# Optimization experiments

Hardware: AMD Instinct MI355X
Metric: run time of the kernel (lower is better)

Reference implementation:

```python
import jax, jax.numpy as jnp
import numpy as np

NUM_HEADS = 16


def _apply_rotary(x, cos, sin):
    # x: [B, H, L, D]; cos/sin: [L, D//2] broadcast over B, H
    d = x.shape[-1] // 2
    x1, x2 = x[..., :d], x[..., d:]
    return jnp.concatenate([x1 * cos - x2 * sin, x2 * cos + x1 * sin], axis=-1)


def setup_inputs() -> dict:
    key = jax.random.key(0)
    k_x, k_c, k_s, k_qkv, k_w, k_b = jax.random.split(key, 6)
    B, L, dim = 2, 2048, 2048
    head_dim = dim // NUM_HEADS
    x = jax.random.normal(k_x, (B, L, dim), dtype=jnp.float32)
    cos = jax.random.uniform(k_c, (L, head_dim // 2), dtype=jnp.float32)
    sin = jax.random.uniform(k_s, (L, head_dim // 2), dtype=jnp.float32)
    scale = 1.0 / np.sqrt(dim)
    w_qkv = jax.random.normal(k_qkv, (dim, 3 * dim), dtype=jnp.float32) * scale
    w_out = jax.random.normal(k_w, (dim, dim), dtype=jnp.float32) * scale
    b_out = jax.random.normal(k_b, (dim,), dtype=jnp.float32) * 0.01
    return {"x": x, "cos": cos, "sin": sin, "w_qkv": w_qkv, "w_out": w_out, "b_out": b_out}


def reference(x, cos, sin, w_qkv, w_out, b_out):
    B, L, dim = x.shape
    H = NUM_HEADS
    D = dim // H
    # fused QKV projection (no bias), split to q,k,v: [B, H, L, D]
    qkv = (x @ w_qkv).reshape(B, L, 3, H, D)
    qkv = jnp.transpose(qkv, (2, 0, 3, 1, 4))
    q, k, v = qkv[0], qkv[1], qkv[2]
    q = _apply_rotary(q, cos, sin)
    k = _apply_rotary(k, cos, sin)
    # scaled dot-product attention (non-causal, scale = 1/sqrt(D))
    scores = jnp.einsum('bhqd,bhkd->bhqk', q, k) / jnp.sqrt(jnp.asarray(D, q.dtype))
    attn = jax.nn.softmax(scores, axis=-1)
    out = jnp.einsum('bhqk,bhkd->bhqd', attn, v)  # [B, H, L, D]
    out = jnp.transpose(out, (0, 2, 1, 3)).reshape(B, L, dim)
    return out @ w_out + b_out
```

## Files before the change

kernel.cpp:

```cpp
#include <hip/hip_runtime.h>
#include <cstdint>
#include <cstddef>

typedef unsigned short u16;
typedef __attribute__((ext_vector_type(2))) unsigned short u16x2;
typedef __attribute__((ext_vector_type(4))) unsigned short u16x4;
typedef __attribute__((ext_vector_type(8))) unsigned short u16x8;
typedef __attribute__((ext_vector_type(4))) float f32x4;
typedef __attribute__((ext_vector_type(8))) __bf16 bf16x8;

#define B_    2
#define L_    2048
#define DIM_  2048
#define H_    16
#define HD_   128
#define NQKV_ 6144
#define M_    4096

__device__ __forceinline__ float b2f(u16 h) {
  union { unsigned u; float f; } v; v.u = ((unsigned)h) << 16; return v.f;
}
__device__ __forceinline__ u16 f2bf(float f) {
  unsigned u = __float_as_uint(f);
  u += 0x7fffu + ((u >> 16) & 1u);
  return (u16)(u >> 16);
}
__device__ __forceinline__ f32x4 mfma16(bf16x8 a, bf16x8 b, f32x4 c) {
  return __builtin_amdgcn_mfma_f32_16x16x32_bf16(a, b, c, 0, 0, 0);
}
__device__ __forceinline__ void async16(const void* g, void* l) {
  __builtin_amdgcn_global_load_lds(
      (const __attribute__((address_space(1))) unsigned*)g,
      (__attribute__((address_space(3))) unsigned*)l, 16, 0, 0);
}

__global__ __launch_bounds__(256) void cvt_bf16(
    const float* __restrict__ src, u16* __restrict__ dst) {
  int i = (blockIdx.x * 256 + threadIdx.x) * 4;
  f32x4 v = *(const f32x4*)&src[i];
  u16x4 o;
  #pragma unroll
  for (int j = 0; j < 4; ++j) o[j] = f2bf(v[j]);
  *(u16x4*)&dst[i] = o;
}

__global__ __launch_bounds__(256) void transpose_cvt(
    const float* __restrict__ src, u16* __restrict__ dst, int R, int C) {
  __shared__ u16 tile[64][66];
  int r0 = blockIdx.y * 64, c0 = blockIdx.x * 64;
  #pragma unroll
  for (int i = 0; i < 16; ++i) {
    int f = i * 256 + threadIdx.x;
    int r = f >> 6, c = f & 63;
    tile[r][c] = f2bf(src[(size_t)(r0 + r) * C + (c0 + c)]);
  }
  __syncthreads();
  #pragma unroll
  for (int i = 0; i < 8; ++i) {
    int f = i * 256 + threadIdx.x;
    int cr = f >> 5, rp = (f & 31) * 2;
    u16x2 v = {tile[rp][cr], tile[rp + 1][cr]};
    *(u16x2*)&dst[(size_t)(c0 + cr) * R + (r0 + rp)] = v;
  }
}

template <int MODE>
__global__ __launch_bounds__(256) void gemm_bt(
    const u16* __restrict__ A, const u16* __restrict__ Bt,
    u16* __restrict__ D0, u16* __restrict__ D1, u16* __restrict__ D2,
    const float* __restrict__ bias, float* __restrict__ outp,
    int M, int N, int K) {
  __shared__ __align__(16) u16 Alds[128 * 32];
  __shared__ __align__(16) u16 Blds[128 * 32];
  const int tid = threadIdx.x;
  const int wave = tid >> 6, lane = tid & 63;
  const int wm = wave >> 1, wn = wave & 1;
  const int ln = lane & 15, qd = lane >> 4;
  const int m0 = blockIdx.y * 128, n0 = blockIdx.x * 128;

  f32x4 acc[4][4];
  #pragma unroll
  for (int i = 0; i < 4; ++i)
    #pragma unroll
    for (int j = 0; j < 4; ++j) acc[i][j] = (f32x4){0.f, 0.f, 0.f, 0.f};

  for (int k0 = 0; k0 < K; k0 += 32) {
    __syncthreads();
    #pragma unroll
    for (int j = 0; j < 2; ++j) {
      int f = (j * 256 + tid) * 8;
      int r = f >> 5, c = f & 31;
      async16(&A[(size_t)(m0 + r) * K + (k0 + c)], &Alds[j * 2048 + wave * 512]);
      async16(&Bt[(size_t)(n0 + r) * K + (k0 + c)], &Blds[j * 2048 + wave * 512]);
    }
    __syncthreads();
    bf16x8 af[4], bfr[4];
    #pragma unroll
    for (int mi = 0; mi < 4; ++mi)
      af[mi] = *(const bf16x8*)&Alds[(wm * 64 + mi * 16 + ln) * 32 + qd * 8];
    #pragma unroll
    for (int ni = 0; ni < 4; ++ni)
      bfr[ni] = *(const bf16x8*)&Blds[(wn * 64 + ni * 16 + ln) * 32 + qd * 8];
    #pragma unroll
    for (int mi = 0; mi < 4; ++mi)
      #pragma unroll
      for (int ni = 0; ni < 4; ++ni)
        acc[mi][ni] = mfma16(af[mi], bfr[ni], acc[mi][ni]);
  }

  #pragma unroll
  for (int mi = 0; mi < 4; ++mi) {
    #pragma unroll
    for (int ni = 0; ni < 4; ++ni) {
      #pragma unroll
      for (int r = 0; r < 4; ++r) {
        int row = m0 + wm * 64 + mi * 16 + qd * 4 + r;
        int col = n0 + wn * 64 + ni * 16 + ln;
        float v = acc[mi][ni][r];
        if (MODE == 2) {
          outp[(size_t)row * N + col] = v + bias[col];
        } else {
          int t = col >> 11;
          int hc = col & 2047;
          int h = hc >> 7, d = hc & 127;
          int b = row >> 11, l = row & 2047;
          u16* dst = (t == 0) ? D0 : ((t == 1) ? D1 : D2);
          dst[((size_t)(b * H_ + h) * L_ + l) * HD_ + d] = f2bf(v);
        }
      }
    }
  }
}

__global__ __launch_bounds__(128) void rotary_k(
    u16* __restrict__ Q, u16* __restrict__ Kb,
    const float* __restrict__ cs, const float* __restrict__ sn) {
  int bid = blockIdx.x;
  int l = bid & (L_ - 1);
  int t = threadIdx.x;
  int d = t & 63;
  u16* P = (t < 64) ? Q : Kb;
  size_t base = (size_t)bid * HD_;
  int ci = l * 64 + d;
  float c = cs[ci], s = sn[ci];
  float x1 = b2f(P[base + d]), x2 = b2f(P[base + d + 64]);
  P[base + d] = f2bf(x1 * c - x2 * s);
  P[base + d + 64] = f2bf(x2 * c + x1 * s);
}

__global__ __launch_bounds__(256) void attn_k(
    const u16* __restrict__ Q, const u16* __restrict__ Kb,
    const u16* __restrict__ V, u16* __restrict__ Ao) {
  __shared__ __align__(16) u16 lds[26624];
  u16* Klds = lds;
  u16* Vlds = lds + 8192;
  u16* Plds = lds + 17408;
  const int tid = threadIdx.x;
  const int w = tid >> 6, lane = tid & 63;
  const int ln = lane & 15, qd = lane >> 4;
  const int qt = blockIdx.x, bh = blockIdx.y;
  const int b = bh >> 4, h = bh & 15;
  const size_t slab = (size_t)bh * (L_ * HD_);
  const int vp = tid & 63, vd0 = 2 * vp;

  #pragma unroll
  for (int j = 0; j < 8; ++j) {
    int oe = j * 2048 + w * 512 + lane * 8;
    int se = oe ^ (((oe >> 7) & 7) << 3);
    async16(&Q[slab + (size_t)qt * 16384 + se], &lds[j * 2048 + w * 512]);
  }
  __syncthreads();
  bf16x8 aq[2][4];
  #pragma unroll
  for (int mi = 0; mi < 2; ++mi) {
    int qrow = w * 32 + mi * 16 + ln;
    #pragma unroll
    for (int kc = 0; kc < 4; ++kc)
      aq[mi][kc] = *(const bf16x8*)&lds[qrow * 128 +
                                        ((kc * 32 + qd * 8) ^ ((qrow & 7) << 3))];
  }

  f32x4 o[2][8];
  #pragma unroll
  for (int i = 0; i < 2; ++i)
    #pragma unroll
    for (int j = 0; j < 8; ++j) o[i][j] = (f32x4){0.f, 0.f, 0.f, 0.f};
  float mst[2][4], lst[2][4];
  #pragma unroll
  for (int i = 0; i < 2; ++i)
    #pragma unroll
    for (int r = 0; r < 4; ++r) { mst[i][r] = -1e30f; lst[i][r] = 0.f; }
  const float SC = 0.12751744f;

  for (int it = 0; it < 32; ++it) {
    unsigned vv[2][8];
    #pragma unroll
    for (int n2 = 0; n2 < 2; ++n2) {
      int key0 = ((tid >> 6) + n2 * 4) * 8;
      #pragma unroll
      for (int e = 0; e < 8; ++e)
        vv[n2][e] = *(const unsigned*)&V[slab + (size_t)(it * 64 + key0 + e) * 128 + vd0];
    }
    __syncthreads();
    #pragma unroll
    for (int j = 0; j < 4; ++j) {
      int oe = j * 2048 + w * 512 + lane * 8;
      int se = oe ^ (((oe >> 7) & 7) << 3);
      async16(&Kb[slab + (size_t)it * 8192 + se], &Klds[j * 2048 + w * 512]);
    }
    #pragma unroll
    for (int n2 = 0; n2 < 2; ++n2) {
      int key0 = ((tid >> 6) + n2 * 4) * 8;
      u16x8 lo, hi;
      #pragma unroll
      for (int e = 0; e < 8; ++e) {
        lo[e] = (u16)(vv[n2][e] & 0xffffu);
        hi[e] = (u16)(vv[n2][e] >> 16);
      }
      *(u16x8*)&Vlds[vd0 * 72 + key0] = lo;
      *(u16x8*)&Vlds[(vd0 + 1) * 72 + key0] = hi;
    }
    __syncthreads();

    f32x4 sa[2][4];
    #pragma unroll
    for (int i = 0; i < 2; ++i)
      #pragma unroll
      for (int j = 0; j < 4; ++j) sa[i][j] = (f32x4){0.f, 0.f, 0.f, 0.f};
    #pragma unroll
    for (int kc = 0; kc < 4; ++kc) {
      bf16x8 bk[4];
      #pragma unroll
      for (int ni = 0; ni < 4; ++ni) {
        int krow = ni * 16 + ln;
        bk[ni] = *(const bf16x8*)&Klds[krow * 128 +
                                       ((kc * 32 + qd * 8) ^ ((krow & 7) << 3))];
      }
      #pragma unroll
      for (int mi = 0; mi < 2; ++mi)
        #pragma unroll
        for (int ni = 0; ni < 4; ++ni)
          sa[mi][ni] = mfma16(aq[mi][kc], bk[ni], sa[mi][ni]);
    }

    #pragma unroll
    for (int mi = 0; mi < 2; ++mi) {
      #pragma unroll
      for (int r = 0; r < 4; ++r) {
        float tmax = -1e30f;
        #pragma unroll
        for (int ni = 0; ni < 4; ++ni) tmax = fmaxf(tmax, sa[mi][ni][r]);
        tmax *= SC;
        tmax = fmaxf(tmax, __shfl_xor(tmax, 1));
        tmax = fmaxf(tmax, __shfl_xor(tmax, 2));
        tmax = fmaxf(tmax, __shfl_xor(tmax, 4));
        tmax = fmaxf(tmax, __shfl_xor(tmax, 8));
        float mnew = fmaxf(mst[mi][r], tmax);
        float alpha = exp2f(mst[mi][r] - mnew);
        float p[4], rs = 0.f;
        #pragma unroll
        for (int ni = 0; ni < 4; ++ni) {
          p[ni] = exp2f(sa[mi][ni][r] * SC - mnew);
          rs += p[ni];
        }
        rs += __shfl_xor(rs, 1);
        rs += __shfl_xor(rs, 2);
        rs += __shfl_xor(rs, 4);
        rs += __shfl_xor(rs, 8);
        lst[mi][r] = lst[mi][r] * alpha + rs;
        mst[mi][r] = mnew;
        #pragma unroll
        for (int di = 0; di < 8; ++di) o[mi][di][r] *= alpha;
        #pragma unroll
        for (int ni = 0; ni < 4; ++ni)
          Plds[(w * 32 + mi * 16 + qd * 4 + r) * 72 + ni * 16 + ln] = f2bf(p[ni]);
      }
    }

    __syncthreads();

    #pragma unroll
    for (int kc = 0; kc < 2; ++kc) {
      bf16x8 ap[2];
      #pragma unroll
      for (int mi = 0; mi < 2; ++mi)
        ap[mi] = *(const bf16x8*)&Plds[(w * 32 + mi * 16 + ln) * 72 + kc * 32 + qd * 8];
      #pragma unroll
      for (int di = 0; di < 8; ++di) {
        bf16x8 bv = *(const bf16x8*)&Vlds[(di * 16 + ln) * 72 + kc * 32 + qd * 8];
        o[0][di] = mfma16(ap[0], bv, o[0][di]);
        o[1][di] = mfma16(ap[1], bv, o[1][di]);
      }
    }
  }

  #pragma unroll
  for (int mi = 0; mi < 2; ++mi) {
    #pragma unroll
    for (int r = 0; r < 4; ++r) {
      float inv = 1.0f / lst[mi][r];
      int lrow = qt * 128 + w * 32 + mi * 16 + qd * 4 + r;
      size_t orow = ((size_t)b * L_ + lrow) * DIM_ + (size_t)h * HD_;
      #pragma unroll
      for (int di = 0; di < 8; ++di)
        Ao[orow + di * 16 + ln] = f2bf(o[mi][di][r] * inv);
    }
  }
}

extern "C" void kernel_launch(void* const* d_in, const int* in_sizes, int n_in,
                              void* d_out, int out_size, void* d_ws, size_t ws_size,
                              hipStream_t stream) {
  const float* x    = (const float*)d_in[0];
  const float* cs   = (const float*)d_in[1];
  const float* sn   = (const float*)d_in[2];
  const float* wqkv = (const float*)d_in[3];
  const float* wout = (const float*)d_in[4];
  const float* bias = (const float*)d_in[5];
  u16* ws = (u16*)d_ws;

  u16* wqkvT = ws;
  u16* woutT = ws;
  u16* xbfAo = wqkvT + 12582912;
  u16* Qb    = xbfAo + 8388608;
  u16* Kbuf  = Qb + 8388608;
  u16* Vbuf  = Kbuf + 8388608;

  cvt_bf16<<<dim3(8192), 256, 0, stream>>>(x, xbfAo);
  transpose_cvt<<<dim3(96, 32), 256, 0, stream>>>(wqkv, wqkvT, 2048, 6144);
  gemm_bt<1><<<dim3(48, 32), 256, 0, stream>>>(
      xbfAo, wqkvT, Qb, Kbuf, Vbuf, nullptr, nullptr, M_, NQKV_, DIM_);
  transpose_cvt<<<dim3(32, 32), 256, 0, stream>>>(wout, woutT, 2048, 2048);
  rotary_k<<<dim3(65536), 128, 0, stream>>>(Qb, Kbuf, cs, sn);
  attn_k<<<dim3(16, 32), 256, 0, stream>>>(Qb, Kbuf, Vbuf, xbfAo);
  gemm_bt<2><<<dim3(16, 32), 256, 0, stream>>>(
      xbfAo, woutT, nullptr, nullptr, nullptr, bias, (float*)d_out, M_, DIM_, DIM_);
}
```

Before: 526.2 us.

## Double-buffer K tiles and prefetch V one iteration ahead in attention

The attention loop now double-buffers K tiles in LDS: the async global-to-LDS load for the next tile is issued while the current tile is consumed. The V rows for the next iteration are also prefetched into registers during the softmax. Padded LDS rows for P and V are replaced by XOR-swizzled layouts, which frees LDS space for the second K buffer. A custom barrier waits only on lgkmcnt, so the wait on the async K loads depends on vmcnt ordering with the V register loads. The changes aim to hide global latency and cut barrier stalls, at the cost of more LDS and register pressure.

```diff
diff --git a/kernel.cpp b/kernel.cpp
--- a/kernel.cpp
+++ b/kernel.cpp
@@ -32,6 +32,12 @@
   __builtin_amdgcn_global_load_lds(
       (const __attribute__((address_space(1))) unsigned*)g,
       (__attribute__((address_space(3))) unsigned*)l, 16, 0, 0);
+}
+__device__ __forceinline__ void barrier_sync() {
+  __builtin_amdgcn_sched_barrier(0);
+  asm volatile("s_waitcnt lgkmcnt(0)" ::: "memory");
+  __builtin_amdgcn_s_barrier();
+  __builtin_amdgcn_sched_barrier(0);
 }
 
 __global__ __launch_bounds__(256) void cvt_bf16(
@@ -151,17 +157,16 @@
 __global__ __launch_bounds__(256) void attn_k(
     const u16* __restrict__ Q, const u16* __restrict__ Kb,
     const u16* __restrict__ V, u16* __restrict__ Ao) {
-  __shared__ __align__(16) u16 lds[26624];
-  u16* Klds = lds;
-  u16* Vlds = lds + 8192;
-  u16* Plds = lds + 17408;
+  __shared__ __align__(16) u16 lds[32768];
+  u16* Vlds = lds + 16384;
+  u16* Plds = lds + 24576;
   const int tid = threadIdx.x;
   const int w = tid >> 6, lane = tid & 63;
   const int ln = lane & 15, qd = lane >> 4;
   const int qt = blockIdx.x, bh = blockIdx.y;
   const int b = bh >> 4, h = bh & 15;
   const size_t slab = (size_t)bh * (L_ * HD_);
-  const int vp = tid & 63, vd0 = 2 * vp;
+  const int vd0 = 2 * lane;
 
   #pragma unroll
   for (int j = 0; j < 8; ++j) {
@@ -179,6 +184,7 @@
       aq[mi][kc] = *(const bf16x8*)&lds[qrow * 128 +
                                         ((kc * 32 + qd * 8) ^ ((qrow & 7) << 3))];
   }
+  __syncthreads();
 
   f32x4 o[2][8];
   #pragma unroll
@@ -192,35 +198,51 @@
     for (int r = 0; r < 4; ++r) { mst[i][r] = -1e30f; lst[i][r] = 0.f; }
   const float SC = 0.12751744f;
 
+  #pragma unroll
+  for (int j = 0; j < 4; ++j) {
+    int oe = j * 2048 + w * 512 + lane * 8;
+    int se = oe ^ (((oe >> 7) & 7) << 3);
+    async16(&Kb[slab + se], &lds[j * 2048 + w * 512]);
+  }
+  unsigned vv[2][8];
+  #pragma unroll
+  for (int n2 = 0; n2 < 2; ++n2) {
+    int key0 = (w + n2 * 4) * 8;
+    #pragma unroll
+    for (int e = 0; e < 8; ++e)
+      vv[n2][e] = *(const unsigned*)&V[slab + (size_t)(key0 + e) * 128 + vd0];
+  }
+
   for (int it = 0; it < 32; ++it) {
-    unsigned vv[2][8];
+    u16* kcur = lds + (it & 1) * 8192;
+    u16* knxt = lds + ((it + 1) & 1) * 8192;
+
+    barrier_sync();
+
+    if (it < 31) {
+      #pragma unroll
+      for (int j = 0; j < 4; ++j) {
+        int oe = j * 2048 + w * 512 + lane * 8;
+        int se = oe ^ (((oe >> 7) & 7) << 3);
+        async16(&Kb[slab + (size_t)(it + 1) * 8192 + se],
+                &knxt[j * 2048 + w * 512]);
+      }
+    }
+
     #pragma unroll
     for (int n2 = 0; n2 < 2; ++n2) {
-      int key0 = ((tid >> 6) + n2 * 4) * 8;
-      #pragma unroll
-      for (int e = 0; e < 8; ++e)
-        vv[n2][e] = *(const unsigned*)&V[slab + (size_t)(it * 64 + key0 + e) * 128 + vd0];
-    }
-    __syncthreads();
-    #pragma unroll
-    for (int j = 0; j < 4; ++j) {
-      int oe = j * 2048 + w * 512 + lane * 8;
-      int se = oe ^ (((oe >> 7) & 7) << 3);
-      async16(&Kb[slab + (size_t)it * 8192 + se], &Klds[j * 2048 + w * 512]);
-    }
-    #pragma unroll
-    for (int n2 = 0; n2 < 2; ++n2) {
-      int key0 = ((tid >> 6) + n2 * 4) * 8;
+      int key0 = (w + n2 * 4) * 8;
       u16x8 lo, hi;
       #pragma unroll
       for (int e = 0; e < 8; ++e) {
         lo[e] = (u16)(vv[n2][e] & 0xffffu);
         hi[e] = (u16)(vv[n2][e] >> 16);
       }
-      *(u16x8*)&Vlds[vd0 * 72 + key0] = lo;
-      *(u16x8*)&Vlds[(vd0 + 1) * 72 + key0] = hi;
-    }
-    __syncthreads();
+      *(u16x8*)&Vlds[vd0 * 64 + (key0 ^ (((vd0 >> 1) & 7) << 3))] = lo;
+      *(u16x8*)&Vlds[(vd0 + 1) * 64 + (key0 ^ (((vd0 >> 1) & 7) << 3))] = hi;
+    }
+
+    barrier_sync();
 
     f32x4 sa[2][4];
     #pragma unroll
@@ -233,7 +255,7 @@
       #pragma unroll
       for (int ni = 0; ni < 4; ++ni) {
         int krow = ni * 16 + ln;
-        bk[ni] = *(const bf16x8*)&Klds[krow * 128 +
+        bk[ni] = *(const bf16x8*)&kcur[krow * 128 +
                                        ((kc * 32 + qd * 8) ^ ((krow & 7) << 3))];
       }
       #pragma unroll
@@ -271,23 +293,40 @@
         mst[mi][r] = mnew;
         #pragma unroll
         for (int di = 0; di < 8; ++di) o[mi][di][r] *= alpha;
+        int prow = w * 32 + mi * 16 + qd * 4 + r;
         #pragma unroll
         for (int ni = 0; ni < 4; ++ni)
-          Plds[(w * 32 + mi * 16 + qd * 4 + r) * 72 + ni * 16 + ln] = f2bf(p[ni]);
-      }
-    }
-
-    __syncthreads();
+          Plds[prow * 64 + ((ni * 16 + ln) ^ ((prow & 7) << 3))] = f2bf(p[ni]);
+      }
+    }
+
+    if (it < 31) {
+      #pragma unroll
+      for (int n2 = 0; n2 < 2; ++n2) {
+        int key0 = (w + n2 * 4) * 8;
+        #pragma unroll
+        for (int e = 0; e < 8; ++e)
+          vv[n2][e] = *(const unsigned*)
+              &V[slab + (size_t)((it + 1) * 64 + key0 + e) * 128 + vd0];
+      }
+    }
+
+    barrier_sync();
 
     #pragma unroll
     for (int kc = 0; kc < 2; ++kc) {
       bf16x8 ap[2];
       #pragma unroll
-      for (int mi = 0; mi < 2; ++mi)
-        ap[mi] = *(const bf16x8*)&Plds[(w * 32 + mi * 16 + ln) * 72 + kc * 32 + qd * 8];
+      for (int mi = 0; mi < 2; ++mi) {
+        int prow = w * 32 + mi * 16 + ln;
+        ap[mi] = *(const bf16x8*)&Plds[prow * 64 +
+                                       ((kc * 32 + qd * 8) ^ ((prow & 7) << 3))];
+      }
       #pragma unroll
       for (int di = 0; di < 8; ++di) {
-        bf16x8 bv = *(const bf16x8*)&Vlds[(di * 16 + ln) * 72 + kc * 32 + qd * 8];
+        int vrow = di * 16 + ln;
+        bf16x8 bv = *(const bf16x8*)&Vlds[vrow * 64 +
+                         ((kc * 32 + qd * 8) ^ (((vrow >> 1) & 7) << 3))];
         o[0][di] = mfma16(ap[0], bv, o[0][di]);
         o[1][di] = mfma16(ap[1], bv, o[1][di]);
       }
```

Result: slower. 615.1 us (+16.9%).
